# Performance work log

Hardware: AMD Instinct MI355X
Metric: run time of the kernel (lower is better)

Reference implementation:

```python
import jax, jax.numpy as jnp
import numpy as np

Q_DIM = 64

def setup_inputs() -> dict:
    key = jax.random.key(0)
    k1, k2, k3, k4 = jax.random.split(key, 4)
    B, T, C, D = 2, 4096, 1024, Q_DIM
    x = jax.random.normal(k1, (B, T, C), dtype=jnp.float32)
    Wq = jax.random.normal(k2, (C, D), dtype=jnp.float32) * (C ** -0.5)
    Wk = jax.random.normal(k3, (C, D), dtype=jnp.float32) * (C ** -0.5)
    Wv = jax.random.normal(k4, (C, D), dtype=jnp.float32) * (C ** -0.5)
    return {"x": x, "Wq": Wq, "Wk": Wk, "Wv": Wv}

def reference(x, Wq, Wk, Wv):
    # x: [B,T,C]; Wq/Wk/Wv: [C,D]
    T = x.shape[1]
    D = Wq.shape[1]
    q = x @ Wq  # [B,T,D]
    k = x @ Wk
    v = x @ Wv
    scale = D ** -0.5
    aff = jnp.einsum('bqd,bkd->bqk', q, k) * scale  # [B,T,T]
    causal = jnp.tril(jnp.ones((T, T), dtype=bool))
    aff = jnp.where(causal, aff, -jnp.inf)
    attn = jax.nn.softmax(aff, axis=-1)
    out = jnp.einsum('bqk,bkd->bqd', attn, v)  # [B,T,D]
    return out
```

## Files before the change

kernel.cpp:

```cpp
#include <hip/hip_runtime.h>

typedef __bf16 bf16_t;
typedef __bf16 bf16x8 __attribute__((ext_vector_type(8)));
typedef __bf16 bf16x4 __attribute__((ext_vector_type(4)));
typedef float  f32x4  __attribute__((ext_vector_type(4)));
typedef _Float16 f16_t;
typedef _Float16 f16x8 __attribute__((ext_vector_type(8)));

#define TSEQ 4096
#define SEGS 8

__global__ __launch_bounds__(256) void wsplit_k(
    const float* __restrict__ Wq, const float* __restrict__ Wk,
    const float* __restrict__ Wv, bf16_t* __restrict__ wT)
{
    __shared__ bf16_t th[64][72];
    const int mat = blockIdx.x >> 4;
    const int kb  = (blockIdx.x & 15) * 64;
    const float* W = (mat == 0) ? Wq : ((mat == 1) ? Wk : Wv);
    const float scale = (mat == 0) ? 0.18033688011112042f : 1.0f;
    const int t  = threadIdx.x;
    const int kl = t >> 2;
    const int dc = (t & 3) * 16;
    #pragma unroll
    for (int i = 0; i < 4; ++i) {
        float4 v = *reinterpret_cast<const float4*>(W + (long)(kb + kl) * 64 + dc + 4 * i);
        th[dc + 4*i + 0][kl] = (bf16_t)(v.x * scale);
        th[dc + 4*i + 1][kl] = (bf16_t)(v.y * scale);
        th[dc + 4*i + 2][kl] = (bf16_t)(v.z * scale);
        th[dc + 4*i + 3][kl] = (bf16_t)(v.w * scale);
    }
    __syncthreads();
    const int d  = t >> 2;
    const int kc = (t & 3) * 16;
    bf16x8 a0 = *reinterpret_cast<const bf16x8*>(&th[d][kc]);
    bf16x8 a1 = *reinterpret_cast<const bf16x8*>(&th[d][kc + 8]);
    long o = (long)(mat * 64 + d) * 1024 + kb + kc;
    *reinterpret_cast<bf16x8*>(wT + o)     = a0;
    *reinterpret_cast<bf16x8*>(wT + o + 8) = a1;
}

__global__ __launch_bounds__(256) void proj_mfma(
    const float* __restrict__ X, const bf16_t* __restrict__ wT,
    bf16_t* __restrict__ qh, bf16_t* __restrict__ kh, bf16_t* __restrict__ vt)
{
    __shared__ __align__(16) unsigned char smem[13824];
    bf16_t (*wl)[48][72] = reinterpret_cast<bf16_t(*)[48][72]>(smem);
    float  (*vtl)[68]    = reinterpret_cast<float(*)[68]>(smem);

    const int tid = threadIdx.x, lane = tid & 63;
    const int mw  = tid >> 6;
    const int q4 = lane & 15, g = lane >> 4;
    const int bx = blockIdx.x;
    const int rg = bx & 127, nb = bx >> 7;
    const long R0 = (long)rg * 64;

    const float* xrow = X + (R0 + 16 * mw + q4) * 1024 + 8 * g;

    const int wrow = tid >> 2, c16 = (tid & 3) * 16;
    const bf16_t* wsrc = wT + (long)(48 * nb + wrow) * 1024 + c16;
    const bool wact = (tid < 192);

    bf16x8 wr0, wr1;
    float4 xE[4], xO[4];
    f32x4 acc[3] = {};

    auto loadW = [&](int t) {
        if (wact) {
            wr0 = *reinterpret_cast<const bf16x8*>(wsrc + t * 64);
            wr1 = *reinterpret_cast<const bf16x8*>(wsrc + t * 64 + 8);
        }
    };
    auto writeW = [&](int buf) {
        if (wact) {
            *reinterpret_cast<bf16x8*>(&wl[buf][wrow][c16])     = wr0;
            *reinterpret_cast<bf16x8*>(&wl[buf][wrow][c16 + 8]) = wr1;
        }
    };
    auto loadX = [&](int t, float4 (&xc)[4]) {
        xc[0] = *reinterpret_cast<const float4*>(xrow + t * 64);
        xc[1] = *reinterpret_cast<const float4*>(xrow + t * 64 + 4);
        xc[2] = *reinterpret_cast<const float4*>(xrow + t * 64 + 32);
        xc[3] = *reinterpret_cast<const float4*>(xrow + t * 64 + 36);
    };

    loadW(0); writeW(0);
    loadW(1);
    loadX(0, xE); loadX(1, xO);
    __syncthreads();

    auto stepf = [&](int t, float4 (&xc)[4]) {
        if (t + 1 < 16) {
            writeW((t + 1) & 1);
            loadW(t + 2 < 16 ? t + 2 : 15);
        }
        bf16x8 a0 = {(bf16_t)xc[0].x, (bf16_t)xc[0].y, (bf16_t)xc[0].z, (bf16_t)xc[0].w,
                     (bf16_t)xc[1].x, (bf16_t)xc[1].y, (bf16_t)xc[1].z, (bf16_t)xc[1].w};
        bf16x8 a1 = {(bf16_t)xc[2].x, (bf16_t)xc[2].y, (bf16_t)xc[2].z, (bf16_t)xc[2].w,
                     (bf16_t)xc[3].x, (bf16_t)xc[3].y, (bf16_t)xc[3].z, (bf16_t)xc[3].w};
        if (t + 2 < 16) loadX(t + 2, xc);
        #pragma unroll
        for (int j = 0; j < 3; ++j) {
            bf16x8 b0 = *reinterpret_cast<const bf16x8*>(&wl[t & 1][16 * j + q4][8 * g]);
            bf16x8 b1 = *reinterpret_cast<const bf16x8*>(&wl[t & 1][16 * j + q4][8 * g + 32]);
            acc[j] = __builtin_amdgcn_mfma_f32_16x16x32_bf16(a0, b0, acc[j], 0, 0, 0);
            acc[j] = __builtin_amdgcn_mfma_f32_16x16x32_bf16(a1, b1, acc[j], 0, 0, 0);
        }
        __syncthreads();
    };
    #pragma unroll
    for (int tt = 0; tt < 16; tt += 2) { stepf(tt, xE); stepf(tt + 1, xO); }

    const int vbase = (nb == 2) ? 0 : 16;
    #pragma unroll
    for (int j = 0; j < 3; ++j) {
        const int nt = 3 * nb + j;
        #pragma unroll
        for (int r = 0; r < 4; ++r) {
            const long row = R0 + 16 * mw + 4 * g + r;
            const float vv = acc[j][r];
            if (nt < 4)      qh[row * 64 + nt * 16 + q4] = (bf16_t)vv;
            else if (nt < 8) kh[row * 64 + (nt - 4) * 16 + q4] = (bf16_t)vv;
            else             vtl[(nt - 8) * 16 + q4 - vbase][16 * mw + 4 * g + r] = vv;
        }
    }
    if (nb >= 2) {
        __syncthreads();
        const int nd = (nb == 2) ? 16 : 48;
        const int dl = tid >> 2, cc = (tid & 3) * 16;
        if (dl < nd) {
            bf16x8 o0, o1;
            #pragma unroll
            for (int i = 0; i < 8; ++i) {
                o0[i] = (bf16_t)vtl[dl][cc + i];
                o1[i] = (bf16_t)vtl[dl][cc + 8 + i];
            }
            bf16_t* dst = vt + (long)(vbase + dl) * 8192 + R0 + cc;
            *reinterpret_cast<bf16x8*>(dst)     = o0;
            *reinterpret_cast<bf16x8*>(dst + 8) = o1;
        }
    }
}

__global__ __launch_bounds__(256) void attn_mfma(
    const bf16_t* __restrict__ qh, const bf16_t* __restrict__ kh,
    const bf16_t* __restrict__ vt,
    f16_t* __restrict__ pO, float* __restrict__ pm, float* __restrict__ pl)
{
    __shared__ __align__(16) unsigned char smem[54272];
    bf16_t (*kl)[64][72]  = reinterpret_cast<bf16_t(*)[64][72]>(smem);
    bf16_t (*vl)[64][72]  = reinterpret_cast<bf16_t(*)[64][72]>(smem + 18432);
    bf16_t (*P)[8][16][8] = reinterpret_cast<bf16_t(*)[8][16][8]>(smem + 36864);
    float  (*ot)[16][68]  = reinterpret_cast<float(*)[16][68]>(smem + 36864);

    const int tid = threadIdx.x, lane = tid & 63, w = tid >> 6;
    const int q4 = lane & 15, g = lane >> 4;
    const int bx = blockIdx.x, b = blockIdx.y;
    const int tile = 63 - (bx >> 3);
    const int seg  = bx & 7;
    const int C = tile + 1;
    if (seg >= C) return;
    const long base = (long)b * TSEQ;
    const int r0 = tile * 64 + 16 * w;

    const bf16_t* qr = qh + (base + r0 + q4) * 64 + 8 * g;
    const bf16x8 qf0 = *reinterpret_cast<const bf16x8*>(qr);
    const bf16x8 qf1 = *reinterpret_cast<const bf16x8*>(qr + 32);

    const int srow = tid >> 2, sc = (tid & 3) * 16;
    const bf16_t* ksrc = kh + (base + srow) * 64 + sc;
    const bf16_t* vsrc = vt + (long)srow * 8192 + base + sc;
    bf16x8 kr0, kr1, vr0, vr1;
    auto loadKV = [&](int kb) {
        kr0 = *reinterpret_cast<const bf16x8*>(ksrc + (long)kb * 64);
        kr1 = *reinterpret_cast<const bf16x8*>(ksrc + (long)kb * 64 + 8);
        vr0 = *reinterpret_cast<const bf16x8*>(vsrc + kb);
        vr1 = *reinterpret_cast<const bf16x8*>(vsrc + kb + 8);
    };
    auto writeKV = [&](int buf) {
        *reinterpret_cast<bf16x8*>(&kl[buf][srow][sc])     = kr0;
        *reinterpret_cast<bf16x8*>(&kl[buf][srow][sc + 8]) = kr1;
        *reinterpret_cast<bf16x8*>(&vl[buf][srow][sc])     = vr0;
        *reinterpret_cast<bf16x8*>(&vl[buf][srow][sc + 8]) = vr1;
    };

    float m = -1e30f, l = 0.f;
    f32x4 oacc[4] = {};

    loadKV(seg << 6);
    writeKV(0);
    { int c1 = seg + SEGS; loadKV((c1 < C ? c1 : seg) << 6); }
    __syncthreads();

    int i = 0;
    for (int c = seg; c < C; c += SEGS, ++i) {
        const int buf = i & 1;
        if (c + SEGS < C) {
            writeKV(buf ^ 1);
            int cn = c + 2 * SEGS;
            loadKV((cn < C ? cn : c + SEGS) << 6);
        }
        const int kb = c << 6;

        f32x4 sacc[4];
        #pragma unroll
        for (int kt = 0; kt < 4; ++kt) {
            bf16x8 kf0 = *reinterpret_cast<const bf16x8*>(&kl[buf][kt * 16 + q4][8 * g]);
            bf16x8 kf1 = *reinterpret_cast<const bf16x8*>(&kl[buf][kt * 16 + q4][8 * g + 32]);
            f32x4 a = {};
            a = __builtin_amdgcn_mfma_f32_16x16x32_bf16(kf0, qf0, a, 0, 0, 0);
            a = __builtin_amdgcn_mfma_f32_16x16x32_bf16(kf1, qf1, a, 0, 0, 0);
            sacc[kt] = a;
        }

        float p[16];
        const bool diag = (c == C - 1);
        float mx = -1e30f;
        #pragma unroll
        for (int kt = 0; kt < 4; ++kt)
            #pragma unroll
            for (int r = 0; r < 4; ++r) {
                float sv = sacc[kt][r];
                if (diag && (kb + kt * 16 + 4 * g + r > r0 + q4)) sv = -1e30f;
                p[kt * 4 + r] = sv;
                mx = fmaxf(mx, sv);
            }
        mx = fmaxf(mx, __shfl_xor(mx, 16));
        mx = fmaxf(mx, __shfl_xor(mx, 32));
        const float mnew = fmaxf(m, mx);
        const float alpha = __builtin_exp2f(m - mnew);
        m = mnew;
        float lsum = 0.f;
        #pragma unroll
        for (int ii = 0; ii < 16; ++ii) { p[ii] = __builtin_exp2f(p[ii] - mnew); lsum += p[ii]; }
        lsum += __shfl_xor(lsum, 16);
        lsum += __shfl_xor(lsum, 32);
        l = l * alpha + lsum;
        #pragma unroll
        for (int dt = 0; dt < 4; ++dt) oacc[dt] *= alpha;

        #pragma unroll
        for (int kt = 0; kt < 4; ++kt) {
            const int cb = 2 * kt + (g >> 1);
            const int ki = (g & 1) << 2;
            bf16x4 hv = {(bf16_t)p[4*kt+0], (bf16_t)p[4*kt+1],
                         (bf16_t)p[4*kt+2], (bf16_t)p[4*kt+3]};
            *reinterpret_cast<bf16x4*>(&P[w][cb][q4][ki]) = hv;
        }
        bf16x8 ph0 = *reinterpret_cast<const bf16x8*>(&P[w][g][q4][0]);
        bf16x8 ph1 = *reinterpret_cast<const bf16x8*>(&P[w][4 + g][q4][0]);
        #pragma unroll
        for (int dt = 0; dt < 4; ++dt) {
            bf16x8 va0 = *reinterpret_cast<const bf16x8*>(&vl[buf][dt * 16 + q4][8 * g]);
            bf16x8 va1 = *reinterpret_cast<const bf16x8*>(&vl[buf][dt * 16 + q4][8 * g + 32]);
            oacc[dt] = __builtin_amdgcn_mfma_f32_16x16x32_bf16(va0, ph0, oacc[dt], 0, 0, 0);
            oacc[dt] = __builtin_amdgcn_mfma_f32_16x16x32_bf16(va1, ph1, oacc[dt], 0, 0, 0);
        }
        __syncthreads();
    }

    const float invl = 1.0f / l;
    #pragma unroll
    for (int dt = 0; dt < 4; ++dt)
        #pragma unroll
        for (int r = 0; r < 4; ++r)
            ot[w][q4][dt * 16 + 4 * g + r] = oacc[dt][r] * invl;

    const long pbase = (((long)b * 64 + tile) * SEGS + seg) * 64;
    {
        const int q  = lane >> 2;
        const int dc = (lane & 3) * 16;
        f16x8 o0, o1;
        #pragma unroll
        for (int ii = 0; ii < 8; ++ii) {
            o0[ii] = (f16_t)ot[w][q][dc + ii];
            o1[ii] = (f16_t)ot[w][q][dc + 8 + ii];
        }
        f16_t* dst = pO + (pbase + 16 * w + q) * 64 + dc;
        *reinterpret_cast<f16x8*>(dst)     = o0;
        *reinterpret_cast<f16x8*>(dst + 8) = o1;
    }
    if (g == 0) {
        pm[pbase + 16 * w + q4] = m;
        pl[pbase + 16 * w + q4] = l;
    }
}

__global__ __launch_bounds__(256) void merge_k(
    const f16_t* __restrict__ pO, const float* __restrict__ pm,
    const float* __restrict__ pl, float* __restrict__ O)
{
    const int tile = blockIdx.x, b = blockIdx.y;
    const int C = tile + 1;
    const int S = (C < SEGS) ? C : SEGS;
    const int t = threadIdx.x;
    const int q = t >> 2, dc = (t & 3) * 16;
    const long pb = ((long)b * 64 + tile) * SEGS;

    float mstar = -1e30f;
    for (int s = 0; s < S; ++s) mstar = fmaxf(mstar, pm[(pb + s) * 64 + q]);
    float L = 0.f;
    float o[16];
    #pragma unroll
    for (int i = 0; i < 16; ++i) o[i] = 0.f;
    for (int s = 0; s < S; ++s) {
        const float ws = __builtin_exp2f(pm[(pb + s) * 64 + q] - mstar) * pl[(pb + s) * 64 + q];
        L += ws;
        const f16_t* src = pO + ((pb + s) * 64 + q) * 64 + dc;
        f16x8 a0 = *reinterpret_cast<const f16x8*>(src);
        f16x8 a1 = *reinterpret_cast<const f16x8*>(src + 8);
        #pragma unroll
        for (int i = 0; i < 8; ++i) {
            o[i]     += ws * (float)a0[i];
            o[8 + i] += ws * (float)a1[i];
        }
    }
    const float inv = 1.0f / L;
    float* dst = O + ((long)b * TSEQ + tile * 64 + q) * 64 + dc;
    #pragma unroll
    for (int i = 0; i < 4; ++i) {
        f32x4 v = {o[4*i] * inv, o[4*i+1] * inv, o[4*i+2] * inv, o[4*i+3] * inv};
        *reinterpret_cast<f32x4*>(dst + 4 * i) = v;
    }
}

extern "C" void kernel_launch(void* const* d_in, const int* in_sizes, int n_in,
                              void* d_out, int out_size, void* d_ws, size_t ws_size,
                              hipStream_t stream)
{
    const float* X  = (const float*)d_in[0];
    const float* Wq = (const float*)d_in[1];
    const float* Wk = (const float*)d_in[2];
    const float* Wv = (const float*)d_in[3];
    float* O = (float*)d_out;

    char* ws = (char*)d_ws;
    size_t off = 0;
    bf16_t* wT = (bf16_t*)(ws + off); off += 192 * 1024 * sizeof(bf16_t);
    bf16_t* qh = (bf16_t*)(ws + off); off += 8192L * 64 * sizeof(bf16_t);
    bf16_t* kh = (bf16_t*)(ws + off); off += 8192L * 64 * sizeof(bf16_t);
    bf16_t* vt = (bf16_t*)(ws + off); off += 64L * 8192 * sizeof(bf16_t);
    f16_t*  pO = (f16_t*)(ws + off);  off += 2L * 64 * SEGS * 64 * 64 * sizeof(f16_t);
    float*  pm = (float*)(ws + off);  off += 2L * 64 * SEGS * 64 * sizeof(float);
    float*  pl = (float*)(ws + off);  off += 2L * 64 * SEGS * 64 * sizeof(float);

    wsplit_k <<<48, 256, 0, stream>>>(Wq, Wk, Wv, wT);
    proj_mfma<<<512, 256, 0, stream>>>(X, wT, qh, kh, vt);
    attn_mfma<<<dim3(512, 2), 256, 0, stream>>>(qh, kh, vt, pO, pm, pl);
    merge_k  <<<dim3(64, 2), 256, 0, stream>>>(pO, pm, pl, O);
}
```

Baseline: 53.76 us.

## Use LDS-only barriers, MFMA priority hints, occupancy bounds and f16 output staging

Replaces __syncthreads with a barrier that waits only on LDS counters (lgkmcnt), so in-flight global prefetches of X/W and K/V can stay outstanding across the barrier. Raises wave priority around MFMA blocks with s_setprio and adds min-blocks-per-CU launch bounds (2 for projection, 3 for attention). Shrinks attention LDS by staging the output tile as f16 instead of f32, which allows vector LDS reads for the epilogue. Correctness depends on the compiler inserting vmcnt waits before the prefetched registers are used, and the tighter launch bounds may force register spills.

New measurement: 52.85 us. Within noise of the previous version (-1.7%).

```diff
diff --git a/kernel.cpp b/kernel.cpp
--- a/kernel.cpp
+++ b/kernel.cpp
@@ -9,6 +9,13 @@
 
 #define TSEQ 4096
 #define SEGS 8
+
+__device__ __forceinline__ void barrier_lds() {
+    __builtin_amdgcn_sched_barrier(0);
+    asm volatile("s_waitcnt lgkmcnt(0)" ::: "memory");
+    __builtin_amdgcn_s_barrier();
+    __builtin_amdgcn_sched_barrier(0);
+}
 
 __global__ __launch_bounds__(256) void wsplit_k(
     const float* __restrict__ Wq, const float* __restrict__ Wk,
@@ -40,7 +47,7 @@
     *reinterpret_cast<bf16x8*>(wT + o + 8) = a1;
 }
 
-__global__ __launch_bounds__(256) void proj_mfma(
+__global__ __launch_bounds__(256, 2) void proj_mfma(
     const float* __restrict__ X, const bf16_t* __restrict__ wT,
     bf16_t* __restrict__ qh, bf16_t* __restrict__ kh, bf16_t* __restrict__ vt)
 {
@@ -87,7 +94,8 @@
     loadW(0); writeW(0);
     loadW(1);
     loadX(0, xE); loadX(1, xO);
-    __syncthreads();
+    asm volatile("" ::: "memory");
+    barrier_lds();
 
     auto stepf = [&](int t, float4 (&xc)[4]) {
         if (t + 1 < 16) {
@@ -99,6 +107,8 @@
         bf16x8 a1 = {(bf16_t)xc[2].x, (bf16_t)xc[2].y, (bf16_t)xc[2].z, (bf16_t)xc[2].w,
                      (bf16_t)xc[3].x, (bf16_t)xc[3].y, (bf16_t)xc[3].z, (bf16_t)xc[3].w};
         if (t + 2 < 16) loadX(t + 2, xc);
+        asm volatile("" ::: "memory");
+        __builtin_amdgcn_s_setprio(1);
         #pragma unroll
         for (int j = 0; j < 3; ++j) {
             bf16x8 b0 = *reinterpret_cast<const bf16x8*>(&wl[t & 1][16 * j + q4][8 * g]);
@@ -106,7 +116,8 @@
             acc[j] = __builtin_amdgcn_mfma_f32_16x16x32_bf16(a0, b0, acc[j], 0, 0, 0);
             acc[j] = __builtin_amdgcn_mfma_f32_16x16x32_bf16(a1, b1, acc[j], 0, 0, 0);
         }
-        __syncthreads();
+        __builtin_amdgcn_s_setprio(0);
+        barrier_lds();
     };
     #pragma unroll
     for (int tt = 0; tt < 16; tt += 2) { stepf(tt, xE); stepf(tt + 1, xO); }
@@ -125,7 +136,7 @@
         }
     }
     if (nb >= 2) {
-        __syncthreads();
+        barrier_lds();
         const int nd = (nb == 2) ? 16 : 48;
         const int dl = tid >> 2, cc = (tid & 3) * 16;
         if (dl < nd) {
@@ -142,16 +153,16 @@
     }
 }
 
-__global__ __launch_bounds__(256) void attn_mfma(
+__global__ __launch_bounds__(256, 3) void attn_mfma(
     const bf16_t* __restrict__ qh, const bf16_t* __restrict__ kh,
     const bf16_t* __restrict__ vt,
     f16_t* __restrict__ pO, float* __restrict__ pm, float* __restrict__ pl)
 {
-    __shared__ __align__(16) unsigned char smem[54272];
+    __shared__ __align__(16) unsigned char smem[46080];
     bf16_t (*kl)[64][72]  = reinterpret_cast<bf16_t(*)[64][72]>(smem);
     bf16_t (*vl)[64][72]  = reinterpret_cast<bf16_t(*)[64][72]>(smem + 18432);
     bf16_t (*P)[8][16][8] = reinterpret_cast<bf16_t(*)[8][16][8]>(smem + 36864);
-    float  (*ot)[16][68]  = reinterpret_cast<float(*)[16][68]>(smem + 36864);
+    f16_t  (*ot)[16][72]  = reinterpret_cast<f16_t(*)[16][72]>(smem + 36864);
 
     const int tid = threadIdx.x, lane = tid & 63, w = tid >> 6;
     const int q4 = lane & 15, g = lane >> 4;
@@ -190,7 +201,8 @@
     loadKV(seg << 6);
     writeKV(0);
     { int c1 = seg + SEGS; loadKV((c1 < C ? c1 : seg) << 6); }
-    __syncthreads();
+    asm volatile("" ::: "memory");
+    barrier_lds();
 
     int i = 0;
     for (int c = seg; c < C; c += SEGS, ++i) {
@@ -199,10 +211,12 @@
             writeKV(buf ^ 1);
             int cn = c + 2 * SEGS;
             loadKV((cn < C ? cn : c + SEGS) << 6);
+            asm volatile("" ::: "memory");
         }
         const int kb = c << 6;
 
         f32x4 sacc[4];
+        __builtin_amdgcn_s_setprio(1);
         #pragma unroll
         for (int kt = 0; kt < 4; ++kt) {
             bf16x8 kf0 = *reinterpret_cast<const bf16x8*>(&kl[buf][kt * 16 + q4][8 * g]);
@@ -212,6 +226,7 @@
             a = __builtin_amdgcn_mfma_f32_16x16x32_bf16(kf1, qf1, a, 0, 0, 0);
             sacc[kt] = a;
         }
+        __builtin_amdgcn_s_setprio(0);
 
         float p[16];
         const bool diag = (c == C - 1);
@@ -249,6 +264,7 @@
         }
         bf16x8 ph0 = *reinterpret_cast<const bf16x8*>(&P[w][g][q4][0]);
         bf16x8 ph1 = *reinterpret_cast<const bf16x8*>(&P[w][4 + g][q4][0]);
+        __builtin_amdgcn_s_setprio(1);
         #pragma unroll
         for (int dt = 0; dt < 4; ++dt) {
             bf16x8 va0 = *reinterpret_cast<const bf16x8*>(&vl[buf][dt * 16 + q4][8 * g]);
@@ -256,7 +272,8 @@
             oacc[dt] = __builtin_amdgcn_mfma_f32_16x16x32_bf16(va0, ph0, oacc[dt], 0, 0, 0);
             oacc[dt] = __builtin_amdgcn_mfma_f32_16x16x32_bf16(va1, ph1, oacc[dt], 0, 0, 0);
         }
-        __syncthreads();
+        __builtin_amdgcn_s_setprio(0);
+        barrier_lds();
     }
 
     const float invl = 1.0f / l;
@@ -264,18 +281,14 @@
     for (int dt = 0; dt < 4; ++dt)
         #pragma unroll
         for (int r = 0; r < 4; ++r)
-            ot[w][q4][dt * 16 + 4 * g + r] = oacc[dt][r] * invl;
+            ot[w][q4][dt * 16 + 4 * g + r] = (f16_t)(oacc[dt][r] * invl);
 
     const long pbase = (((long)b * 64 + tile) * SEGS + seg) * 64;
     {
         const int q  = lane >> 2;
         const int dc = (lane & 3) * 16;
-        f16x8 o0, o1;
-        #pragma unroll
-        for (int ii = 0; ii < 8; ++ii) {
-            o0[ii] = (f16_t)ot[w][q][dc + ii];
-            o1[ii] = (f16_t)ot[w][q][dc + 8 + ii];
-        }
+        f16x8 o0 = *reinterpret_cast<const f16x8*>(&ot[w][q][dc]);
+        f16x8 o1 = *reinterpret_cast<const f16x8*>(&ot[w][q][dc + 8]);
         f16_t* dst = pO + (pbase + 16 * w + q) * 64 + dc;
         *reinterpret_cast<f16x8*>(dst)     = o0;
         *reinterpret_cast<f16x8*>(dst + 8) = o1;
```
